# Kernel tuning notes

Hardware: AMD Instinct MI355X
Metric: run time of the kernel (lower is better)

Reference implementation:

```python
import jax, jax.numpy as jnp
import numpy as np

N, F_IN, F_OUT, HEADS = 4096, 128, 64, 4


def setup_inputs() -> dict:
    key = jax.random.key(0)
    k1, k2, k3, k4, k5 = jax.random.split(key, 5)
    X = jax.random.normal(k1, (N, F_IN), dtype=jnp.float32)
    A = jax.random.randint(k2, (N, N), 0, 2, dtype=jnp.int32)
    # zero the diagonal: the torch loop always prepends the self node, so the
    # adjacency must not also contain it (would duplicate the self term).
    A = A * (1 - jnp.eye(N, dtype=jnp.int32))
    # per-head Linear(F_IN, F_OUT) weights/bias and Linear(2*F_OUT, 1, bias=False)
    W = jax.random.normal(k3, (HEADS, F_OUT, F_IN), dtype=jnp.float32) / np.sqrt(F_IN)
    b = jax.random.normal(k4, (HEADS, F_OUT), dtype=jnp.float32) * 0.02
    att = jax.random.normal(k5, (HEADS, 2 * F_OUT), dtype=jnp.float32) / np.sqrt(2 * F_OUT)
    return {"X": X, "A": A, "W": W, "b": b, "att": att}


def reference(X, A, W, b, att):
    # H[h, n, o] = line_h(X)
    H = jnp.einsum('nf,hof->hno', X, W) + b[:, None, :]
    f_out = W.shape[1]
    a_src, a_dst = att[:, :f_out], att[:, f_out:]
    # score e_ij = leaky_relu(a_src.H_i + a_dst.H_j)
    s = jnp.einsum('hno,ho->hn', H, a_src)  # query-side term (xi_bar expanded)
    d = jnp.einsum('hno,ho->hn', H, a_dst)  # neighbor-side term
    e = jax.nn.leaky_relu(s[:, :, None] + d[:, None, :])  # [H, N, N]
    # neighbor set = {self} U {j : A_ij != 0}
    mask = (A > 0) | jnp.eye(A.shape[0], dtype=bool)
    e = jnp.where(mask[None], e, -jnp.inf)
    alpha = jax.nn.softmax(e, axis=-1)  # segment softmax per node row
    # weighted sum per head, then mean over heads (sum / head in the original)
    out = jnp.einsum('hnm,hmo->no', alpha, H) / W.shape[0]
    return out  # [N, F_OUT]
```

## Files before the change

kernel.cpp:

```cpp
#include <hip/hip_runtime.h>
#include <hip/hip_bf16.h>


#define NN 4096
#define FIN 128
#define FOUT 64
#define NH 4

typedef __attribute__((ext_vector_type(8))) short bf16x8;
typedef __attribute__((ext_vector_type(4))) float f32x4;
typedef __attribute__((ext_vector_type(4))) unsigned int u32x4;

__device__ __forceinline__ unsigned short f32_bf16(float f) {
    unsigned u = __builtin_bit_cast(unsigned, f);
    u += 0x7fffu + ((u >> 16) & 1u);
    return (unsigned short)(u >> 16);
}

__device__ __forceinline__ void gload16(const void* g, void* l) {
    __builtin_amdgcn_global_load_lds(
        (const __attribute__((address_space(1))) unsigned*)g,
        (__attribute__((address_space(3))) unsigned*)l, 16, 0, 0);
}

__global__ __launch_bounds__(256) void pack_bits(
    const int* __restrict__ A, unsigned long long* __restrict__ Abits)
{
    const int row  = blockIdx.x;
    const int lane = threadIdx.x & 63;
    const int wv   = threadIdx.x >> 6;
    const int* arow = A + (size_t)row * NN;
    #pragma unroll 4
    for (int c = 0; c < 16; ++c) {
        const int col = c * 256 + wv * 64 + lane;
        unsigned long long m = __ballot(__builtin_nontemporal_load(&arow[col]) > 0);
        if (lane == 0) Abits[(size_t)row * 64 + c * 4 + wv] = m;
    }
}

__global__ __launch_bounds__(256) void gat_prep(
    const float* __restrict__ X, const float* __restrict__ W,
    const float* __restrict__ b, const float* __restrict__ att,
    unsigned short* __restrict__ HbfT, float* __restrict__ Hrow,
    float* __restrict__ s_out, float* __restrict__ d_out,
    float* __restrict__ es_g, float* __restrict__ es2_g,
    float* __restrict__ ed_g, float* __restrict__ ed2_g)
{
    const int rb = blockIdx.x;
    const int h  = blockIdx.y;
    const int n0 = rb * 32;
    const int t  = threadIdx.x;

    __shared__ float Xl[32][132];
    __shared__ float Wt[128][68];

    for (int g = t; g < 32 * 32; g += 256) {
        int row = g >> 5, c4 = g & 31;
        float4 v = *(const float4*)&X[(size_t)(n0 + row) * FIN + c4 * 4];
        *(float4*)&Xl[row][c4 * 4] = v;
    }
    for (int g = t; g < 64 * 32; g += 256) {
        int o = g >> 5, c4 = g & 31;
        float4 v = *(const float4*)&W[((size_t)h * FOUT + o) * FIN + c4 * 4];
        Wt[c4 * 4 + 0][o] = v.x; Wt[c4 * 4 + 1][o] = v.y;
        Wt[c4 * 4 + 2][o] = v.z; Wt[c4 * 4 + 3][o] = v.w;
    }
    __syncthreads();

    const int rg = t >> 4;
    const int og = t & 15;
    float acc[2][4] = {};

    #pragma unroll 4
    for (int f4 = 0; f4 < 32; ++f4) {
        float xv[2][4], wv[4][4];
        #pragma unroll
        for (int i = 0; i < 2; ++i) {
            float4 tmp = *(const float4*)&Xl[rg * 2 + i][f4 * 4];
            xv[i][0] = tmp.x; xv[i][1] = tmp.y; xv[i][2] = tmp.z; xv[i][3] = tmp.w;
        }
        #pragma unroll
        for (int k = 0; k < 4; ++k) {
            float4 tmp = *(const float4*)&Wt[f4 * 4 + k][og * 4];
            wv[k][0] = tmp.x; wv[k][1] = tmp.y; wv[k][2] = tmp.z; wv[k][3] = tmp.w;
        }
        #pragma unroll
        for (int i = 0; i < 2; ++i)
            #pragma unroll
            for (int k = 0; k < 4; ++k)
                #pragma unroll
                for (int jj = 0; jj < 4; ++jj)
                    acc[i][jj] = fmaf(xv[i][k], wv[k][jj], acc[i][jj]);
    }

    float bb[4], as_[4], ad_[4];
    #pragma unroll
    for (int jj = 0; jj < 4; ++jj) {
        bb[jj]  = b[h * FOUT + og * 4 + jj];
        as_[jj] = att[h * 2 * FOUT + og * 4 + jj];
        ad_[jj] = att[h * 2 * FOUT + FOUT + og * 4 + jj];
    }
    #pragma unroll
    for (int i = 0; i < 2; ++i)
        #pragma unroll
        for (int jj = 0; jj < 4; ++jj)
            acc[i][jj] += bb[jj];

    float sp[2] = {0.f, 0.f}, dp[2] = {0.f, 0.f};
    #pragma unroll
    for (int i = 0; i < 2; ++i)
        #pragma unroll
        for (int jj = 0; jj < 4; ++jj) {
            sp[i] = fmaf(acc[i][jj], as_[jj], sp[i]);
            dp[i] = fmaf(acc[i][jj], ad_[jj], dp[i]);
        }
    #pragma unroll
    for (int off = 1; off < 16; off <<= 1) {
        #pragma unroll
        for (int i = 0; i < 2; ++i) {
            sp[i] += __shfl_xor(sp[i], off);
            dp[i] += __shfl_xor(dp[i], off);
        }
    }
    if (og == 0) {
        #pragma unroll
        for (int i = 0; i < 2; ++i) {
            int nn = n0 + rg * 2 + i;
            s_out[h * NN + nn]  = sp[i];
            d_out[h * NN + nn]  = dp[i];
            es_g [h * NN + nn]  = __expf(sp[i]);
            es2_g[h * NN + nn]  = __expf(0.01f * sp[i]);
            ed_g [h * NN + nn]  = __expf(dp[i]);
            ed2_g[h * NN + nn]  = __expf(0.01f * dp[i]);
        }
    }

    #pragma unroll
    for (int i = 0; i < 2; ++i) {
        float4 v = make_float4(acc[i][0], acc[i][1], acc[i][2], acc[i][3]);
        *(float4*)&Hrow[((size_t)h * NN + n0 + rg * 2 + i) * FOUT + og * 4] = v;
    }
    #pragma unroll
    for (int jj = 0; jj < 4; ++jj) {
        int o = og * 4 + jj;
        ushort2 p;
        p.x = f32_bf16(acc[0][jj]);
        p.y = f32_bf16(acc[1][jj]);
        *(ushort2*)&HbfT[((size_t)h * FOUT + o) * NN + n0 + rg * 2] = p;
    }
}

struct SMem {
    union {
        __align__(16) unsigned short H[3][64][128];
        struct {
            float red[6][16][68];
            float redl[6][16];
        } fin;
    };
    unsigned bits[3][32][4];
    float ed [3][128];
    float ed2[3][128];
};

__global__ __launch_bounds__(512, 4) void gat_main(
    const unsigned* __restrict__ Abits, const unsigned short* __restrict__ HbfT,
    const float* __restrict__ s_g, const float* __restrict__ d_g,
    const float* __restrict__ es_g, const float* __restrict__ es2_g,
    const float* __restrict__ ed_g, const float* __restrict__ ed2_g,
    const float* __restrict__ Hrow, float* __restrict__ outH)
{
    const int id   = blockIdx.x;
    const int h    = id & 3;
    const int tile = id >> 2;
    const int n0   = tile * 32;
    const int tid  = threadIdx.x;
    const int w    = tid >> 6;
    const int lane = tid & 63;
    const int r    = lane & 15;
    const int q    = lane >> 4;
    const int qs   = q * 8;
    const int rg   = w & 1;
    const int kg   = w >> 1;

    __shared__ SMem sm;

    const int nrow = n0 + rg * 16 + r;
    const float es  = es_g [h * NN + nrow];
    const float es2 = es2_g[h * NN + nrow];

    const int sblk = ((kg * 4 + q) ^ r) & 15;

    const int rowA = 8 * w + (lane >> 4);
    const int rowB = rowA + 4;
    const int blkL = lane & 15;
    const unsigned short* gH0 =
        HbfT + ((size_t)(h * FOUT) + rowA) * NN + (size_t)(blkL ^ (rowA & 15)) * 8;
    const unsigned short* gH1 =
        HbfT + ((size_t)(h * FOUT) + rowB) * NN + (size_t)(blkL ^ (rowB & 15)) * 8;
    const unsigned* gBits = Abits + (size_t)(n0 + lane) * 128;
    const float*    gEd   = ed_g  + (size_t)h * NN + lane * 4;
    const float*    gEd2  = ed2_g + (size_t)h * NN + lane * 4;

    bf16x8 ones;
    #pragma unroll
    for (int i = 0; i < 8; ++i) ones[i] = (short)0x3F80;

    f32x4 acc0 = {0,0,0,0}, acc1 = {0,0,0,0}, acc2 = {0,0,0,0},
          acc3 = {0,0,0,0}, accl = {0,0,0,0};

    auto STAGE = [&](int chn, int bt) {
        const size_t coff = (size_t)chn * 128;
        gload16(gH0 + coff, &sm.H[bt][8 * w][0]);
        gload16(gH1 + coff, &sm.H[bt][8 * w + 4][0]);
        if      (w == 3) { if (lane < 32) gload16(gBits + (size_t)chn * 4, &sm.bits[bt][0][0]); }
        else if (w == 4) { if (lane < 32) gload16(gEd   + coff,            &sm.ed [bt][0]); }
        else if (w == 5) { if (lane < 32) gload16(gEd2  + coff,            &sm.ed2[bt][0]); }
    };

    auto COMPUTE = [&](int bc) {
        const unsigned bits8 = sm.bits[bc][rg * 16 + r][kg] >> qs;
        const float4 e0 = *(const float4*)&sm.ed [bc][kg * 32 + qs];
        const float4 e1 = *(const float4*)&sm.ed [bc][kg * 32 + qs + 4];
        const float4 g0 = *(const float4*)&sm.ed2[bc][kg * 32 + qs];
        const float4 g1 = *(const float4*)&sm.ed2[bc][kg * 32 + qs + 4];
        const float edv [8] = {e0.x, e0.y, e0.z, e0.w, e1.x, e1.y, e1.z, e1.w};
        const float ed2v[8] = {g0.x, g0.y, g0.z, g0.w, g1.x, g1.y, g1.z, g1.w};
        u32x4 afu;
        #pragma unroll
        for (int p = 0; p < 4; ++p) {
            const int j0 = 2 * p, j1 = 2 * p + 1;
            float wa = (bits8 & (1u << j0))
                     ? fmaxf(es * edv[j0], es2 * ed2v[j0]) : 0.0f;
            float wb = (bits8 & (1u << j1))
                     ? fmaxf(es * edv[j1], es2 * ed2v[j1]) : 0.0f;
            __hip_bfloat162 pk = __float22bfloat162_rn(make_float2(wa, wb));
            unsigned u;
            __builtin_memcpy(&u, &pk, sizeof(u));
            afu[p] = u;
        }
        const bf16x8 af = __builtin_bit_cast(bf16x8, afu);

        const bf16x8 b0 = *(const bf16x8*)&sm.H[bc][r     ][sblk * 8];
        const bf16x8 b1 = *(const bf16x8*)&sm.H[bc][r + 16][sblk * 8];
        const bf16x8 b2 = *(const bf16x8*)&sm.H[bc][r + 32][sblk * 8];
        const bf16x8 b3 = *(const bf16x8*)&sm.H[bc][r + 48][sblk * 8];

        acc0 = __builtin_amdgcn_mfma_f32_16x16x32_bf16(af, b0,   acc0, 0, 0, 0);
        acc1 = __builtin_amdgcn_mfma_f32_16x16x32_bf16(af, b1,   acc1, 0, 0, 0);
        acc2 = __builtin_amdgcn_mfma_f32_16x16x32_bf16(af, b2,   acc2, 0, 0, 0);
        acc3 = __builtin_amdgcn_mfma_f32_16x16x32_bf16(af, b3,   acc3, 0, 0, 0);
        accl = __builtin_amdgcn_mfma_f32_16x16x32_bf16(af, ones, accl, 0, 0, 0);
    };

    STAGE(0, 0);
    STAGE(1, 1);

    int bc = 0;
    for (int ch = 0; ch < 31; ++ch) {
        if (w >= 3 && w <= 5) asm volatile("s_waitcnt vmcnt(3)" ::: "memory");
        else                  asm volatile("s_waitcnt vmcnt(2)" ::: "memory");
        __builtin_amdgcn_s_barrier();
        if (ch + 2 < 32) {
            int bt = bc + 2; if (bt >= 3) bt -= 3;
            STAGE(ch + 2, bt);
        }
        COMPUTE(bc);
        bc = (bc == 2) ? 0 : bc + 1;
    }
    asm volatile("s_waitcnt vmcnt(0)" ::: "memory");
    __builtin_amdgcn_s_barrier();
    COMPUTE(bc);

    __syncthreads();

    if (kg > 0) {
        const int widx = (kg - 1) * 2 + rg;
        #pragma unroll
        for (int reg = 0; reg < 4; ++reg) {
            const int rr = q * 4 + reg;
            sm.fin.red[widx][rr][ 0 + r] = acc0[reg];
            sm.fin.red[widx][rr][16 + r] = acc1[reg];
            sm.fin.red[widx][rr][32 + r] = acc2[reg];
            sm.fin.red[widx][rr][48 + r] = acc3[reg];
        }
        if (r == 0) {
            #pragma unroll
            for (int reg = 0; reg < 4; ++reg)
                sm.fin.redl[widx][q * 4 + reg] = accl[reg];
        }
    }
    __syncthreads();
    if (kg == 0) {
        #pragma unroll
        for (int kk = 0; kk < 3; ++kk) {
            const int widx = kk * 2 + rg;
            #pragma unroll
            for (int reg = 0; reg < 4; ++reg) {
                const int rr = q * 4 + reg;
                acc0[reg] += sm.fin.red[widx][rr][ 0 + r];
                acc1[reg] += sm.fin.red[widx][rr][16 + r];
                acc2[reg] += sm.fin.red[widx][rr][32 + r];
                acc3[reg] += sm.fin.red[widx][rr][48 + r];
                accl[reg] += sm.fin.redl[widx][rr];
            }
        }
        #pragma unroll
        for (int reg = 0; reg < 4; ++reg) {
            const int rr  = q * 4 + reg;
            const int nn2 = n0 + rg * 16 + rr;
            const float tt = s_g[h * NN + nn2] + d_g[h * NN + nn2];
            const float wd = __expf(fmaxf(tt, 0.01f * tt));
            const float inv = 0.25f / (accl[reg] + wd);
            const float* hr = &Hrow[((size_t)h * NN + nn2) * FOUT];
            float*       ob = &outH[((size_t)h * NN + nn2) * FOUT];
            ob[ 0 + r] = (acc0[reg] + wd * hr[ 0 + r]) * inv;
            ob[16 + r] = (acc1[reg] + wd * hr[16 + r]) * inv;
            ob[32 + r] = (acc2[reg] + wd * hr[32 + r]) * inv;
            ob[48 + r] = (acc3[reg] + wd * hr[48 + r]) * inv;
        }
    }
}

__global__ __launch_bounds__(256) void gat_fin(
    const float* __restrict__ outH, float* __restrict__ out)
{
    const int i = blockIdx.x * 256 + threadIdx.x;
    const f32x4* p = (const f32x4*)outH;
    f32x4 v0 = __builtin_nontemporal_load(p + i);
    f32x4 v1 = __builtin_nontemporal_load(p + i +  65536);
    f32x4 v2 = __builtin_nontemporal_load(p + i + 131072);
    f32x4 v3 = __builtin_nontemporal_load(p + i + 196608);
    f32x4 s = (v0 + v1) + (v2 + v3);
    *((f32x4*)out + i) = s;
}

extern "C" void kernel_launch(void* const* d_in, const int* in_sizes, int n_in,
                              void* d_out, int out_size, void* d_ws, size_t ws_size,
                              hipStream_t stream) {
    const float* X   = (const float*)d_in[0];
    const int*   A   = (const int*)  d_in[1];
    const float* W   = (const float*)d_in[2];
    const float* b   = (const float*)d_in[3];
    const float* att = (const float*)d_in[4];
    float* out = (float*)d_out;

    char* ws = (char*)d_ws;
    unsigned short* HbfT = (unsigned short*)ws;
    size_t off = (size_t)NH * FOUT * NN * 2;
    float* s_buf   = (float*)(ws + off);  off += (size_t)NH * NN * 4;
    float* d_buf   = (float*)(ws + off);  off += (size_t)NH * NN * 4;
    float* es_buf  = (float*)(ws + off);  off += (size_t)NH * NN * 4;
    float* es2_buf = (float*)(ws + off);  off += (size_t)NH * NN * 4;
    float* ed_buf  = (float*)(ws + off);  off += (size_t)NH * NN * 4;
    float* ed2_buf = (float*)(ws + off);  off += (size_t)NH * NN * 4;
    unsigned long long* Abits = (unsigned long long*)(ws + off);
    off += (size_t)NN * 64 * 8;
    float* Hrow   = (float*)(ws + off);
    off += (size_t)NH * NN * FOUT * 4;
    float* outH   = (float*)(ws + off);
    off += (size_t)NH * NN * FOUT * 4;

    pack_bits<<<NN, 256, 0, stream>>>(A, Abits);
    gat_prep<<<dim3(128, 4), 256, 0, stream>>>(X, W, b, att, HbfT, Hrow,
                                               s_buf, d_buf,
                                               es_buf, es2_buf, ed_buf, ed2_buf);
    gat_main<<<512, 512, 0, stream>>>((const unsigned*)Abits, HbfT,
                                      s_buf, d_buf,
                                      es_buf, es2_buf, ed_buf, ed2_buf,
                                      Hrow, outH);
    gat_fin<<<256, 256, 0, stream>>>(outH, out);
}
```

Before: 161.8 us.

## Split neighbor dimension across two blocks and merge partials in finalize kernel

```diff
diff --git a/kernel.cpp b/kernel.cpp
--- a/kernel.cpp
+++ b/kernel.cpp
@@ -152,28 +152,29 @@
 
 struct SMem {
     union {
-        __align__(16) unsigned short H[3][64][128];
+        __align__(16) unsigned short H[2][64][128];
         struct {
             float red[6][16][68];
             float redl[6][16];
         } fin;
     };
-    unsigned bits[3][32][4];
-    float ed [3][128];
-    float ed2[3][128];
+    unsigned bits[2][32][4];
+    float ed [2][128];
+    float ed2[2][128];
 };
 
-__global__ __launch_bounds__(512, 4) void gat_main(
+__global__ __launch_bounds__(512, 6) void gat_main(
     const unsigned* __restrict__ Abits, const unsigned short* __restrict__ HbfT,
-    const float* __restrict__ s_g, const float* __restrict__ d_g,
     const float* __restrict__ es_g, const float* __restrict__ es2_g,
     const float* __restrict__ ed_g, const float* __restrict__ ed2_g,
-    const float* __restrict__ Hrow, float* __restrict__ outH)
+    float* __restrict__ Hpart, float* __restrict__ lpart)
 {
     const int id   = blockIdx.x;
     const int h    = id & 3;
-    const int tile = id >> 2;
+    const int half = (id >> 2) & 1;
+    const int tile = id >> 3;
     const int n0   = tile * 32;
+    const int c0   = half * 2048;
     const int tid  = threadIdx.x;
     const int w    = tid >> 6;
     const int lane = tid & 63;
@@ -195,12 +196,12 @@
     const int rowB = rowA + 4;
     const int blkL = lane & 15;
     const unsigned short* gH0 =
-        HbfT + ((size_t)(h * FOUT) + rowA) * NN + (size_t)(blkL ^ (rowA & 15)) * 8;
+        HbfT + ((size_t)(h * FOUT) + rowA) * NN + c0 + (size_t)(blkL ^ (rowA & 15)) * 8;
     const unsigned short* gH1 =
-        HbfT + ((size_t)(h * FOUT) + rowB) * NN + (size_t)(blkL ^ (rowB & 15)) * 8;
-    const unsigned* gBits = Abits + (size_t)(n0 + lane) * 128;
-    const float*    gEd   = ed_g  + (size_t)h * NN + lane * 4;
-    const float*    gEd2  = ed2_g + (size_t)h * NN + lane * 4;
+        HbfT + ((size_t)(h * FOUT) + rowB) * NN + c0 + (size_t)(blkL ^ (rowB & 15)) * 8;
+    const unsigned* gBits = Abits + (size_t)(n0 + lane) * 128 + half * 64;
+    const float*    gEd   = ed_g  + (size_t)h * NN + c0 + lane * 4;
+    const float*    gEd2  = ed2_g + (size_t)h * NN + c0 + lane * 4;
 
     bf16x8 ones;
     #pragma unroll
@@ -214,8 +215,8 @@
         gload16(gH0 + coff, &sm.H[bt][8 * w][0]);
         gload16(gH1 + coff, &sm.H[bt][8 * w + 4][0]);
         if      (w == 3) { if (lane < 32) gload16(gBits + (size_t)chn * 4, &sm.bits[bt][0][0]); }
-        else if (w == 4) { if (lane < 32) gload16(gEd   + coff,            &sm.ed [bt][0]); }
-        else if (w == 5) { if (lane < 32) gload16(gEd2  + coff,            &sm.ed2[bt][0]); }
+        else if (w == 4) { if (lane < 32) gload16(gEd  + coff, &sm.ed [bt][0]); }
+        else if (w == 5) { if (lane < 32) gload16(gEd2 + coff, &sm.ed2[bt][0]); }
     };
 
     auto COMPUTE = [&](int bc) {
@@ -254,25 +255,14 @@
     };
 
     STAGE(0, 0);
-    STAGE(1, 1);
-
-    int bc = 0;
-    for (int ch = 0; ch < 31; ++ch) {
-        if (w >= 3 && w <= 5) asm volatile("s_waitcnt vmcnt(3)" ::: "memory");
-        else                  asm volatile("s_waitcnt vmcnt(2)" ::: "memory");
-        __builtin_amdgcn_s_barrier();
-        if (ch + 2 < 32) {
-            int bt = bc + 2; if (bt >= 3) bt -= 3;
-            STAGE(ch + 2, bt);
-        }
-        COMPUTE(bc);
-        bc = (bc == 2) ? 0 : bc + 1;
-    }
-    asm volatile("s_waitcnt vmcnt(0)" ::: "memory");
-    __builtin_amdgcn_s_barrier();
-    COMPUTE(bc);
-
     __syncthreads();
+
+    for (int ch = 0; ch < 16; ++ch) {
+        const int buf = ch & 1;
+        if (ch < 15) STAGE(ch + 1, buf ^ 1);
+        COMPUTE(buf);
+        __syncthreads();
+    }
 
     if (kg > 0) {
         const int widx = (kg - 1) * 2 + rg;
@@ -305,34 +295,45 @@
                 accl[reg] += sm.fin.redl[widx][rr];
             }
         }
+        float* hb = Hpart + ((size_t)(half * NH + h) * NN + n0 + rg * 16) * FOUT;
         #pragma unroll
         for (int reg = 0; reg < 4; ++reg) {
-            const int rr  = q * 4 + reg;
-            const int nn2 = n0 + rg * 16 + rr;
-            const float tt = s_g[h * NN + nn2] + d_g[h * NN + nn2];
-            const float wd = __expf(fmaxf(tt, 0.01f * tt));
-            const float inv = 0.25f / (accl[reg] + wd);
-            const float* hr = &Hrow[((size_t)h * NN + nn2) * FOUT];
-            float*       ob = &outH[((size_t)h * NN + nn2) * FOUT];
-            ob[ 0 + r] = (acc0[reg] + wd * hr[ 0 + r]) * inv;
-            ob[16 + r] = (acc1[reg] + wd * hr[16 + r]) * inv;
-            ob[32 + r] = (acc2[reg] + wd * hr[32 + r]) * inv;
-            ob[48 + r] = (acc3[reg] + wd * hr[48 + r]) * inv;
-        }
-    }
-}
-
-__global__ __launch_bounds__(256) void gat_fin(
-    const float* __restrict__ outH, float* __restrict__ out)
+            const int rr = q * 4 + reg;
+            hb[rr * FOUT +  0 + r] = acc0[reg];
+            hb[rr * FOUT + 16 + r] = acc1[reg];
+            hb[rr * FOUT + 32 + r] = acc2[reg];
+            hb[rr * FOUT + 48 + r] = acc3[reg];
+        }
+        if (r == 0) {
+            #pragma unroll
+            for (int reg = 0; reg < 4; ++reg)
+                lpart[(size_t)(half * NH + h) * NN + n0 + rg * 16 + q * 4 + reg] = accl[reg];
+        }
+    }
+}
+
+__global__ __launch_bounds__(128) void gat_fin(
+    const float* __restrict__ Hpart, const float* __restrict__ Hrow,
+    const float* __restrict__ lpart, const float* __restrict__ s_g,
+    const float* __restrict__ d_g, float* __restrict__ out)
 {
-    const int i = blockIdx.x * 256 + threadIdx.x;
-    const f32x4* p = (const f32x4*)outH;
-    f32x4 v0 = __builtin_nontemporal_load(p + i);
-    f32x4 v1 = __builtin_nontemporal_load(p + i +  65536);
-    f32x4 v2 = __builtin_nontemporal_load(p + i + 131072);
-    f32x4 v3 = __builtin_nontemporal_load(p + i + 196608);
-    f32x4 s = (v0 + v1) + (v2 + v3);
-    *((f32x4*)out + i) = s;
+    const int i = blockIdx.x * 128 + threadIdx.x;
+    const int n = i >> 4;
+    const int o = (i & 15) * 4;
+
+    f32x4 res = {0.f, 0.f, 0.f, 0.f};
+    #pragma unroll
+    for (int h = 0; h < NH; ++h) {
+        const float l = lpart[(size_t)h * NN + n] + lpart[(size_t)(NH + h) * NN + n];
+        const float tt = s_g[h * NN + n] + d_g[h * NN + n];
+        const float wd = __expf(fmaxf(tt, 0.01f * tt));
+        const float inv = 0.25f / (l + wd);
+        f32x4 p0 = *(const f32x4*)&Hpart[((size_t)h * NN + n) * FOUT + o];
+        f32x4 p1 = *(const f32x4*)&Hpart[((size_t)(NH + h) * NN + n) * FOUT + o];
+        f32x4 hr = *(const f32x4*)&Hrow[((size_t)h * NN + n) * FOUT + o];
+        res += (p0 + p1 + wd * hr) * inv;
+    }
+    *(f32x4*)&out[(size_t)n * FOUT + o] = res;
 }
 
 extern "C" void kernel_launch(void* const* d_in, const int* in_sizes, int n_in,
@@ -358,16 +359,17 @@
     off += (size_t)NN * 64 * 8;
     float* Hrow   = (float*)(ws + off);
     off += (size_t)NH * NN * FOUT * 4;
-    float* outH   = (float*)(ws + off);
-    off += (size_t)NH * NN * FOUT * 4;
+    float* Hpart  = (float*)(ws + off);
+    off += (size_t)2 * NH * NN * FOUT * 4;
+    float* lpart  = (float*)(ws + off);
+    off += (size_t)2 * NH * NN * 4;
 
     pack_bits<<<NN, 256, 0, stream>>>(A, Abits);
     gat_prep<<<dim3(128, 4), 256, 0, stream>>>(X, W, b, att, HbfT, Hrow,
                                                s_buf, d_buf,
                                                es_buf, es2_buf, ed_buf, ed2_buf);
-    gat_main<<<512, 512, 0, stream>>>((const unsigned*)Abits, HbfT,
-                                      s_buf, d_buf,
-                                      es_buf, es2_buf, ed_buf, ed2_buf,
-                                      Hrow, outH);
-    gat_fin<<<256, 256, 0, stream>>>(outH, out);
-}
+    gat_main<<<1024, 512, 0, stream>>>((const unsigned*)Abits, HbfT,
+                                       es_buf, es2_buf, ed_buf, ed2_buf,
+                                       Hpart, lpart);
+    gat_fin<<<512, 128, 0, stream>>>(Hpart, Hrow, lpart, s_buf, d_buf, out);
+}
```

After: 157.5 us. -2.6%, faster.
